# Performance work log

Hardware: AMD Instinct MI355X
Metric: run time of the kernel (lower is better)

## Reference

```python
import jax, jax.numpy as jnp
import numpy as np

GRID_H = 128
GRID_W = 128
D = 64
K = 16
HID = 4 * D
EPS = 1e-5


def _hankel_filters(L, k):
    # Hankel matrix Z[i,j] = 2 / ((i+j)^3 - (i+j)), 1-indexed; top-k eigvecs scaled by eigval^0.25
    idx = np.arange(1, L + 1)
    s = (idx[:, None] + idx[None, :]).astype(np.float64)
    Z = 2.0 / (s ** 3 - s)
    vals, vecs = np.linalg.eigh(Z)
    phi = vecs[:, -k:] * (vals[-k:] ** 0.25)
    return jnp.asarray(phi, dtype=jnp.float32)  # (L, k)


def setup_inputs() -> dict:
    key = jax.random.key(0)
    ks = jax.random.split(key, 9)
    def n(k, shape, scale=0.02):
        return jax.random.normal(k, shape, dtype=jnp.float32) * scale
    return {
        'v': jax.random.normal(ks[0], (4, GRID_H * GRID_W, D), dtype=jnp.float32),
        'gamma_row': jnp.ones((D,), jnp.float32), 'beta_row': jnp.zeros((D,), jnp.float32),
        'gamma_col': jnp.ones((D,), jnp.float32), 'beta_col': jnp.zeros((D,), jnp.float32),
        'm_plus_row': n(ks[1], (K, D, D)), 'm_minus_row': n(ks[2], (K, D, D)),
        'm_plus_col': n(ks[3], (K, D, D)), 'm_minus_col': n(ks[4], (K, D, D)),
        'w1_row': n(ks[5], (D, HID)), 'b1_row': jnp.zeros((HID,), jnp.float32),
        'w2_row': n(ks[6], (HID, D)), 'b2_row': jnp.zeros((D,), jnp.float32),
        'w1_col': n(ks[7], (D, HID)), 'b1_col': jnp.zeros((HID,), jnp.float32),
        'w2_col': n(ks[8], (HID, D)), 'b2_col': jnp.zeros((D,), jnp.float32),
        'phi_row': _hankel_filters(GRID_W, K),
        'phi_col': _hankel_filters(GRID_H, K),
    }


def _layernorm(x, g, b):
    mu = jnp.mean(x, -1, keepdims=True)
    var = jnp.mean((x - mu) ** 2, -1, keepdims=True)
    return (x - mu) * jax.lax.rsqrt(var + EPS) * g + b


def _ministu(x, phi, mp, mm, w1, b1, w2, b2):
    # x: (B, L, d); phi: (L, K). Causal FFT conv with pos/neg featurization, then per-filter projection + MLP.
    B, L, d = x.shape
    nfft = 2 * L
    sgn = jnp.where(jnp.arange(L) % 2 == 0, 1.0, -1.0).astype(x.dtype)  # (-1)^t
    pf = jnp.fft.rfft(phi, n=nfft, axis=0)                         # (F, K)
    xf = jnp.fft.rfft(x, n=nfft, axis=1)                           # (B, F, d)
    xmf = jnp.fft.rfft(x * sgn[None, :, None], n=nfft, axis=1)     # (B, F, d)
    up = jnp.fft.irfft(pf[None, :, :, None] * xf[:, :, None, :], n=nfft, axis=1)[:, :L]   # (B, L, K, d)
    um = jnp.fft.irfft(pf[None, :, :, None] * xmf[:, :, None, :], n=nfft, axis=1)[:, :L]
    um = um * sgn[None, :, None, None]
    spec = jnp.einsum('blkd,kde->ble', up, mp) + jnp.einsum('blkd,kde->ble', um, mm)
    h = jax.nn.gelu(spec @ w1 + b1)
    return h @ w2 + b2


def reference(v, gamma_row, beta_row, gamma_col, beta_col,
              m_plus_row, m_minus_row, m_plus_col, m_minus_col,
              w1_row, b1_row, w2_row, b2_row,
              w1_col, b1_col, w2_col, b2_col,
              phi_row, phi_col):
    B, N, d = v.shape
    x = v.reshape(B, GRID_H, GRID_W, d)
    # row pass: (B*H, W, d)
    xr = x.reshape(B * GRID_H, GRID_W, d)
    xr = xr + _ministu(_layernorm(xr, gamma_row, beta_row), phi_row,
                       m_plus_row, m_minus_row, w1_row, b1_row, w2_row, b2_row)
    x = xr.reshape(B, GRID_H, GRID_W, d).transpose(0, 2, 1, 3)
    # col pass: (B*W, H, d)
    xc = x.reshape(B * GRID_W, GRID_H, d)
    xc = xc + _ministu(_layernorm(xc, gamma_col, beta_col), phi_col,
                       m_plus_col, m_minus_col, w1_col, b1_col, w2_col, b2_col)
    x = xc.reshape(B, GRID_W, GRID_H, d).transpose(0, 2, 1, 3)
    return x.reshape(B, N, d)
```

## Files before the change

kernel.cpp:

```cpp
#include <hip/hip_runtime.h>
#include <hip/hip_fp8.h>

typedef __attribute__((ext_vector_type(8))) short bf16x8;
typedef __attribute__((ext_vector_type(4))) float f32x4;
typedef __attribute__((ext_vector_type(8))) int i32x8;
typedef __attribute__((ext_vector_type(4))) unsigned int u32x4;

__device__ __forceinline__ float gelu_fast(float x) {
    const float u = 0.7978845608028654f * x * (1.0f + 0.044715f * x * x);
    return x * __builtin_amdgcn_rcpf(1.0f + __expf(-2.0f * u));
}

__device__ __forceinline__ unsigned short f2bf(float x) {
    union { float f; unsigned int u; } v; v.f = x;
    unsigned int r = v.u + 0x7FFF + ((v.u >> 16) & 1);
    return (unsigned short)(r >> 16);
}

__device__ __forceinline__ unsigned char f2fp8(float x) {
    __hip_fp8_e4m3 h(x);
    return *(unsigned char*)&h;
}

__global__ __launch_bounds__(256) void init_kernel(const float* __restrict__ phi_r, const float* __restrict__ mp_r,
                                                   const float* __restrict__ mm_r, unsigned char* __restrict__ GfR,
                                                   const float* __restrict__ phi_c, const float* __restrict__ mp_c,
                                                   const float* __restrict__ mm_c, unsigned char* __restrict__ GfC,
                                                   const float* __restrict__ w1r, const float* __restrict__ w1c,
                                                   const float* __restrict__ w2r, const float* __restrict__ w2c,
                                                   unsigned short* __restrict__ w1tr, unsigned short* __restrict__ w1tc,
                                                   unsigned short* __restrict__ w2tr, unsigned short* __restrict__ w2tc) {
    const int bid = blockIdx.x, tid = threadIdx.x;
    __shared__ float phis[256];
    __shared__ unsigned char tile8[4096];
    if (bid < 256) {
        const int side = bid >> 7, rem = bid & 127;
        const int chunk = rem >> 3, s0 = (rem & 7) * 16;
        const float* phi = side ? phi_c : phi_r;
        const float* mp  = side ? mp_c  : mp_r;
        const float* mm  = side ? mm_c  : mm_r;
        unsigned char* Gf8 = side ? GfC : GfR;
        const int i = chunk * 256 + tid;
        float pe[16], po[16];
#pragma unroll
        for (int k = 0; k < 16; ++k) {
            const float a = mp[k * 4096 + i];
            const float b = mm[k * 4096 + i];
            pe[k] = a + b; po[k] = a - b;
        }
        phis[tid] = phi[s0 * 16 + tid];
        __syncthreads();
        const int e = tid & 63, dl = tid >> 6;
        const int d0 = chunk * 4;
#pragma unroll
        for (int sb = 0; sb < 16; ++sb) {
            const int s = s0 + sb;
            const float* pk = &phis[sb * 16];
            float acc = 0.0f;
            if (s & 1) {
#pragma unroll
                for (int k = 0; k < 16; ++k) acc += pk[k] * po[k];
            } else {
#pragma unroll
                for (int k = 0; k < 16; ++k) acc += pk[k] * pe[k];
            }
            tile8[sb * 256 + e * 4 + dl] = f2fp8(acc * 32.0f);
        }
        __syncthreads();
#pragma unroll
        for (int it = 0; it < 4; ++it) {
            const int p = it * 256 + tid;
            const int sb = p >> 6, ee = p & 63;
            unsigned int v = *(const unsigned int*)&tile8[sb * 256 + ee * 4];
            const int s = s0 + sb;
            const int sp = s >> 1, hi = s & 1;
            const int k0 = 64 * hi + d0;
            const int gg = k0 >> 5, kk0 = k0 & 31;
            *(unsigned int*)&Gf8[(size_t)sp * 8192 + (ee >> 4) * 2048 +
                                 ((ee & 15) + 16 * gg) * 32 + kk0] = v;
        }
    } else {
        const int b = bid - 256;
        if (b < 2) {
            const float* w1 = b ? w1c : w1r;
            unsigned short* dst = b ? w1tc : w1tr;
            const int n = tid;
            for (int k = 0; k < 64; ++k) dst[n * 64 + k] = f2bf(w1[k * 256 + n]);
        } else {
            const float* w2 = (b == 3) ? w2c : w2r;
            unsigned short* dst = (b == 3) ? w2tc : w2tr;
            const int n = tid & 63, kq = tid >> 6;
            for (int kk2 = 0; kk2 < 64; ++kk2) {
                const int k = kq * 64 + kk2;
                dst[n * 256 + k] = f2bf(w2[k * 64 + n]);
            }
        }
    }
}

#define SPEC_BODY(RR, BC, BN)                                                        \
    {                                                                                \
        const int sp_ = 4 * (RR) + w;                                                \
        if ((RR) < 15) {                                                             \
            const unsigned char* gq = Gf8 + (size_t)(sp_ + 4) * 8192 + lane * 32;    \
            _Pragma("unroll")                                                        \
            for (int f = 0; f < 4; ++f) BN[f] = *(const i32x8*)(gq + f * 2048);      \
        }                                                                            \
        const int jmin_ = __builtin_amdgcn_readfirstlane((2 * sp_ + 1) >> 4);        \
        __builtin_amdgcn_s_setprio(1);                                               \
        _Pragma("unroll")                                                            \
        for (int j = 0; j < 8; ++j) {                                                \
            if (j >= jmin_) {                                                        \
                const int srow = 16 + 16 * j - 2 * sp_ - (g >> 1) + m;               \
                const int cb_ = 2 * (g & 1);                                         \
                u32x4 lo_ = *(const u32x4*)&lds8[srow * 64 + ((cb_ ^ (srow & 3)) << 4)];       \
                u32x4 hi_ = *(const u32x4*)&lds8[srow * 64 + (((cb_ + 1) ^ (srow & 3)) << 4)]; \
                i32x8 av;                                                            \
                av[0] = lo_[0]; av[1] = lo_[1]; av[2] = lo_[2]; av[3] = lo_[3];      \
                av[4] = hi_[0]; av[5] = hi_[1]; av[6] = hi_[2]; av[7] = hi_[3];      \
                _Pragma("unroll")                                                    \
                for (int nt = 0; nt < 4; ++nt)                                       \
                    acc[j][nt] = __builtin_amdgcn_mfma_scale_f32_16x16x128_f8f6f4(   \
                        av, BC[nt], acc[j][nt], 0, 0, 0, 0x7F7F7F7F, 0, 0x7F7F7F7F); \
            }                                                                        \
        }                                                                            \
        __builtin_amdgcn_s_setprio(0);                                               \
    }

__global__ __launch_bounds__(256, 2) void fused_kernel(const float* __restrict__ xin,
                                                       float* __restrict__ xout,
                                                       const unsigned char* __restrict__ Gf8,
                                                       const unsigned short* __restrict__ w1t,
                                                       const unsigned short* __restrict__ w2t,
                                                       const float* __restrict__ b1,
                                                       const float* __restrict__ b2,
                                                       const float* __restrict__ gamma,
                                                       const float* __restrict__ beta,
                                                       int rmul, int tmul) {
    __shared__ unsigned char lds8[51200];
    unsigned short* const ldsu = (unsigned short*)lds8;
    const int tid = threadIdx.x;
    const int w = tid >> 6, lane = tid & 63;
    const int seq = blockIdx.x;
    const int m = lane & 15, g = lane >> 4;
    const int bb = seq >> 7, rr = seq & 127;
    const size_t base = (size_t)bb * 1048576 + (size_t)rr * (size_t)rmul;

    *(unsigned int*)&lds8[tid * 4] = 0u;

    i32x8 Ba[4], Bb[4];
    {
        const unsigned char* gq = Gf8 + (size_t)w * 8192 + lane * 32;
#pragma unroll
        for (int f = 0; f < 4; ++f) Ba[f] = *(const i32x8*)(gq + f * 2048);
    }

    {
        const float gl = gamma[lane], bl = beta[lane];
        float xv[32];
#pragma unroll
        for (int ti = 0; ti < 32; ++ti)
            xv[ti] = xin[base + (size_t)(w * 32 + ti) * tmul + lane];
#pragma unroll
        for (int ti = 0; ti < 32; ++ti) {
            const int t = w * 32 + ti;
            float s1 = xv[ti];
#pragma unroll
            for (int mm2 = 32; mm2 >= 1; mm2 >>= 1) s1 += __shfl_xor(s1, mm2);
            const float mu = s1 * (1.0f / 64.0f);
            const float dv = xv[ti] - mu;
            float s2 = dv * dv;
#pragma unroll
            for (int mm2 = 32; mm2 >= 1; mm2 >>= 1) s2 += __shfl_xor(s2, mm2);
            const float rstd = rsqrtf(s2 * (1.0f / 64.0f) + 1e-5f);
            const float nv = dv * rstd * gl + bl;
            lds8[(t + 16) * 64 + (((lane >> 4) ^ (t & 3)) << 4) + (lane & 15)] = f2fp8(nv);
        }
    }
    __syncthreads();

    f32x4 acc[8][4];
#pragma unroll
    for (int j = 0; j < 8; ++j)
#pragma unroll
        for (int nt = 0; nt < 4; ++nt) {
            f32x4 z = {0.0f, 0.0f, 0.0f, 0.0f};
            acc[j][nt] = z;
        }
    for (int rp = 0; rp < 8; ++rp) {
        SPEC_BODY(2 * rp,     Ba, Bb);
        SPEC_BODY(2 * rp + 1, Bb, Ba);
    }

    char* const scrA = (char*)lds8 + 18432;
    char* const scrB = (char*)lds8 + 34816;
    if (w == 1 || w == 3) {
        char* pb = (w == 1 ? scrA : scrB) + lane * 16;
#pragma unroll
        for (int j = 0; j < 4; ++j)
#pragma unroll
            for (int nt = 0; nt < 4; ++nt)
                *(f32x4*)(pb + (j * 4 + nt) * 1024) = acc[j][nt];
    }
    bf16x8 bw1a[2][2], bw1b[2][2];
    float b1va[2], b1vb[2];
#pragma unroll
    for (int nt = 0; nt < 2; ++nt) {
        const int col0 = w * 32 + nt * 16 + m;
#pragma unroll
        for (int j = 0; j < 2; ++j) {
            bw1a[nt][j] = *(const bf16x8*)&w1t[col0 * 64 + (4 * j + g) * 8];
            bw1b[nt][j] = *(const bf16x8*)&w1t[(128 + col0) * 64 + (4 * j + g) * 8];
        }
        b1va[nt] = b1[col0];
        b1vb[nt] = b1[128 + col0];
    }
    __syncthreads();
    if (w == 0 || w == 2) {
        const char* pb = (w == 0 ? scrA : scrB) + lane * 16;
#pragma unroll
        for (int j = 0; j < 4; ++j)
#pragma unroll
            for (int nt = 0; nt < 4; ++nt)
                acc[j][nt] += *(const f32x4*)(pb + (j * 4 + nt) * 1024);
    }
    __syncthreads();
    if (w == 1 || w == 3) {
        char* pb = (w == 1 ? scrA : scrB) + lane * 16;
#pragma unroll
        for (int j = 4; j < 8; ++j)
#pragma unroll
            for (int nt = 0; nt < 4; ++nt)
                *(f32x4*)(pb + ((j - 4) * 4 + nt) * 1024) = acc[j][nt];
    }
    __syncthreads();
    if (w == 0 || w == 2) {
        const char* pb = (w == 0 ? scrA : scrB) + lane * 16;
#pragma unroll
        for (int j = 4; j < 8; ++j)
#pragma unroll
            for (int nt = 0; nt < 4; ++nt)
                acc[j][nt] += *(const f32x4*)(pb + ((j - 4) * 4 + nt) * 1024);
        if (w == 0) {
#pragma unroll
            for (int j = 4; j < 8; ++j)
#pragma unroll
                for (int nt = 0; nt < 4; ++nt)
                    *(f32x4*)(scrA + ((j - 4) * 4 + nt) * 1024 + lane * 16) = acc[j][nt];
        } else {
#pragma unroll
            for (int j = 0; j < 4; ++j)
#pragma unroll
                for (int nt = 0; nt < 4; ++nt)
                    *(f32x4*)(scrB + (j * 4 + nt) * 1024 + lane * 16) = acc[j][nt];
        }
    }
    __syncthreads();
    if (w == 0) {
#pragma unroll
        for (int j = 0; j < 4; ++j)
#pragma unroll
            for (int nt = 0; nt < 4; ++nt) {
                acc[j][nt] += *(const f32x4*)(scrB + (j * 4 + nt) * 1024 + lane * 16);
#pragma unroll
                for (int rv = 0; rv < 4; ++rv) {
                    const int row = j * 16 + 4 * g + rv;
                    const int col = nt * 16 + m;
                    ldsu[row * 64 + (((col >> 3) ^ (row & 7)) << 3) + (col & 7)] = f2bf(acc[j][nt][rv] * 0.03125f);
                }
            }
    } else if (w == 2) {
#pragma unroll
        for (int j = 4; j < 8; ++j)
#pragma unroll
            for (int nt = 0; nt < 4; ++nt) {
                acc[j][nt] += *(const f32x4*)(scrA + ((j - 4) * 4 + nt) * 1024 + lane * 16);
#pragma unroll
                for (int rv = 0; rv < 4; ++rv) {
                    const int row = j * 16 + 4 * g + rv;
                    const int col = nt * 16 + m;
                    ldsu[row * 64 + (((col >> 3) ^ (row & 7)) << 3) + (col & 7)] = f2bf(acc[j][nt][rv] * 0.03125f);
                }
            }
    }
    __syncthreads();

    float xr[2][4][4];
#pragma unroll
    for (int mt = 0; mt < 2; ++mt)
#pragma unroll
        for (int nt = 0; nt < 4; ++nt)
#pragma unroll
            for (int rv = 0; rv < 4; ++rv)
                xr[mt][nt][rv] = xin[base + (size_t)((w + 4 * mt) * 16 + 4 * g + rv) * tmul + nt * 16 + m];

    float b2v[4];
#pragma unroll
    for (int nt = 0; nt < 4; ++nt) b2v[nt] = b2[nt * 16 + m];
    f32x4 acc2[2][4];
#pragma unroll
    for (int mt = 0; mt < 2; ++mt)
#pragma unroll
        for (int nt = 0; nt < 4; ++nt) {
            f32x4 z = {b2v[nt], b2v[nt], b2v[nt], b2v[nt]};
            acc2[mt][nt] = z;
        }

#pragma unroll
    for (int half = 0; half < 2; ++half) {
        f32x4 acc1[8][2];
#pragma unroll
        for (int mt = 0; mt < 8; ++mt)
#pragma unroll
            for (int nt = 0; nt < 2; ++nt) {
                const float bv = half ? b1vb[nt] : b1va[nt];
                f32x4 z = {bv, bv, bv, bv};
                acc1[mt][nt] = z;
            }
        __builtin_amdgcn_s_setprio(1);
#pragma unroll
        for (int mt = 0; mt < 8; ++mt) {
            const int row = mt * 16 + m;
            const int c0 = (g ^ (row & 7)) << 3;
            bf16x8 a0 = *(const bf16x8*)&ldsu[row * 64 + c0];
            bf16x8 a1 = *(const bf16x8*)&ldsu[row * 64 + (c0 ^ 32)];
#pragma unroll
            for (int nt = 0; nt < 2; ++nt) {
                const bf16x8 w0f = half ? bw1b[nt][0] : bw1a[nt][0];
                const bf16x8 w1f = half ? bw1b[nt][1] : bw1a[nt][1];
                acc1[mt][nt] = __builtin_amdgcn_mfma_f32_16x16x32_bf16(a0, w0f, acc1[mt][nt], 0, 0, 0);
                acc1[mt][nt] = __builtin_amdgcn_mfma_f32_16x16x32_bf16(a1, w1f, acc1[mt][nt], 0, 0, 0);
            }
        }
        __builtin_amdgcn_s_setprio(0);
#pragma unroll
        for (int mt = 0; mt < 8; ++mt)
#pragma unroll
            for (int nt = 0; nt < 2; ++nt) {
                const int col = w * 32 + nt * 16 + m;
                const int c = col >> 3, jj = col & 7;
#pragma unroll
                for (int rv = 0; rv < 4; ++rv) {
                    const int row = mt * 16 + 4 * g + rv;
                    ldsu[8192 + row * 128 + ((c ^ (row & 7)) << 3) + jj] = f2bf(gelu_fast(acc1[mt][nt][rv]));
                }
            }
        __syncthreads();

        __builtin_amdgcn_s_setprio(1);
#pragma unroll
        for (int j = 0; j < 4; ++j) {
            bf16x8 aa[2];
#pragma unroll
            for (int mt = 0; mt < 2; ++mt) {
                const int row = (w + 4 * mt) * 16 + m;
                aa[mt] = *(const bf16x8*)&ldsu[8192 + row * 128 + (((4 * j + g) ^ (row & 7)) << 3)];
            }
#pragma unroll
            for (int nt = 0; nt < 4; ++nt) {
                const int row = nt * 16 + m;
                bf16x8 bfr = *(const bf16x8*)&w2t[row * 256 + half * 128 + (4 * j + g) * 8];
                acc2[0][nt] = __builtin_amdgcn_mfma_f32_16x16x32_bf16(aa[0], bfr, acc2[0][nt], 0, 0, 0);
                acc2[1][nt] = __builtin_amdgcn_mfma_f32_16x16x32_bf16(aa[1], bfr, acc2[1][nt], 0, 0, 0);
            }
        }
        __builtin_amdgcn_s_setprio(0);
        if (half == 0) __syncthreads();
    }

#pragma unroll
    for (int mt = 0; mt < 2; ++mt)
#pragma unroll
        for (int nt = 0; nt < 4; ++nt)
#pragma unroll
            for (int rv = 0; rv < 4; ++rv) {
                const int row = (w + 4 * mt) * 16 + 4 * g + rv;
                const int col = nt * 16 + m;
                const size_t xi = base + (size_t)row * tmul + col;
                xout[xi] = xr[mt][nt][rv] + acc2[mt][nt][rv];
            }
}

extern "C" void kernel_launch(void* const* d_in, const int* in_sizes, int n_in,
                              void* d_out, int out_size, void* d_ws, size_t ws_size,
                              hipStream_t stream) {
    const float* v         = (const float*)d_in[0];
    const float* gamma_row = (const float*)d_in[1];
    const float* beta_row  = (const float*)d_in[2];
    const float* gamma_col = (const float*)d_in[3];
    const float* beta_col  = (const float*)d_in[4];
    const float* mp_row    = (const float*)d_in[5];
    const float* mm_row    = (const float*)d_in[6];
    const float* mp_col    = (const float*)d_in[7];
    const float* mm_col    = (const float*)d_in[8];
    const float* w1_row    = (const float*)d_in[9];
    const float* b1_row    = (const float*)d_in[10];
    const float* w2_row    = (const float*)d_in[11];
    const float* b2_row    = (const float*)d_in[12];
    const float* w1_col    = (const float*)d_in[13];
    const float* b1_col    = (const float*)d_in[14];
    const float* w2_col    = (const float*)d_in[15];
    const float* b2_col    = (const float*)d_in[16];
    const float* phi_row   = (const float*)d_in[17];
    const float* phi_col   = (const float*)d_in[18];
    float* out = (float*)d_out;
    char* ws   = (char*)d_ws;

    unsigned char* GfR   = (unsigned char*)ws;
    unsigned char* GfC   = (unsigned char*)(ws + (1u << 20));
    unsigned short* w1tR = (unsigned short*)(ws + (2u << 20));
    unsigned short* w2tR = (unsigned short*)(ws + (2u << 20) + 32768);
    unsigned short* w1tC = (unsigned short*)(ws + (2u << 20) + 65536);
    unsigned short* w2tC = (unsigned short*)(ws + (2u << 20) + 98304);

    init_kernel<<<260, 256, 0, stream>>>(phi_row, mp_row, mm_row, GfR,
                                         phi_col, mp_col, mm_col, GfC,
                                         w1_row, w1_col, w2_row, w2_col,
                                         w1tR, w1tC, w2tR, w2tC);

    fused_kernel<<<512, 256, 0, stream>>>(v, out, GfR, w1tR, w2tR, b1_row, b2_row,
                                          gamma_row, beta_row, 8192, 64);
    fused_kernel<<<512, 256, 0, stream>>>(out, out, GfC, w1tC, w2tC, b1_col, b2_col,
                                          gamma_col, beta_col, 64, 8192);
}
```

Before: 100.1 us.

## Partition spectral MFMA work by output row tiles instead of filter slices

Each wave now owns two output row tiles (w and 7-w) and loops over all filter positions sp needed for those rows, rather than splitting the sp range across waves and accumulating all eight tiles. This removes the multi-stage cross-wave LDS reduction, several barriers and the 8x4 accumulator array, which cuts register pressure. The pairing of a short and a long tile is meant to balance the triangular causal work across waves. Each wave now loads all G slices itself, so global/L2 traffic for the fp8 filter operands goes up.

```diff
diff --git a/kernel.cpp b/kernel.cpp
--- a/kernel.cpp
+++ b/kernel.cpp
@@ -98,31 +98,40 @@
     }
 }
 
-#define SPEC_BODY(RR, BC, BN)                                                        \
+#define SPEC_BODY(SP, BC, BN)                                                        \
     {                                                                                \
-        const int sp_ = 4 * (RR) + w;                                                \
-        if ((RR) < 15) {                                                             \
-            const unsigned char* gq = Gf8 + (size_t)(sp_ + 4) * 8192 + lane * 32;    \
+        const int sp_ = (SP);                                                        \
+        if (sp_ + 2 <= spmax) {                                                      \
+            const unsigned char* gq = Gf8 + (size_t)(sp_ + 2) * 8192 + lane * 32;    \
             _Pragma("unroll")                                                        \
             for (int f = 0; f < 4; ++f) BN[f] = *(const i32x8*)(gq + f * 2048);      \
         }                                                                            \
-        const int jmin_ = __builtin_amdgcn_readfirstlane((2 * sp_ + 1) >> 4);        \
         __builtin_amdgcn_s_setprio(1);                                               \
-        _Pragma("unroll")                                                            \
-        for (int j = 0; j < 8; ++j) {                                                \
-            if (j >= jmin_) {                                                        \
-                const int srow = 16 + 16 * j - 2 * sp_ - (g >> 1) + m;               \
-                const int cb_ = 2 * (g & 1);                                         \
-                u32x4 lo_ = *(const u32x4*)&lds8[srow * 64 + ((cb_ ^ (srow & 3)) << 4)];       \
-                u32x4 hi_ = *(const u32x4*)&lds8[srow * 64 + (((cb_ + 1) ^ (srow & 3)) << 4)]; \
-                i32x8 av;                                                            \
-                av[0] = lo_[0]; av[1] = lo_[1]; av[2] = lo_[2]; av[3] = lo_[3];      \
-                av[4] = hi_[0]; av[5] = hi_[1]; av[6] = hi_[2]; av[7] = hi_[3];      \
-                _Pragma("unroll")                                                    \
-                for (int nt = 0; nt < 4; ++nt)                                       \
-                    acc[j][nt] = __builtin_amdgcn_mfma_scale_f32_16x16x128_f8f6f4(   \
-                        av, BC[nt], acc[j][nt], 0, 0, 0, 0x7F7F7F7F, 0, 0x7F7F7F7F); \
-            }                                                                        \
+        {                                                                            \
+            const int srow = 16 + 16 * j2 - 2 * sp_ - (g >> 1) + m;                  \
+            const int cb_ = 2 * (g & 1);                                             \
+            u32x4 lo_ = *(const u32x4*)&lds8[srow * 64 + ((cb_ ^ (srow & 3)) << 4)];       \
+            u32x4 hi_ = *(const u32x4*)&lds8[srow * 64 + (((cb_ + 1) ^ (srow & 3)) << 4)]; \
+            i32x8 av;                                                                \
+            av[0] = lo_[0]; av[1] = lo_[1]; av[2] = lo_[2]; av[3] = lo_[3];          \
+            av[4] = hi_[0]; av[5] = hi_[1]; av[6] = hi_[2]; av[7] = hi_[3];          \
+            _Pragma("unroll")                                                        \
+            for (int nt = 0; nt < 4; ++nt)                                           \
+                acc[1][nt] = __builtin_amdgcn_mfma_scale_f32_16x16x128_f8f6f4(       \
+                    av, BC[nt], acc[1][nt], 0, 0, 0, 0x7F7F7F7F, 0, 0x7F7F7F7F);     \
+        }                                                                            \
+        if (sp_ <= 8 * w + 7) {                                                      \
+            const int srow = 16 + 16 * w - 2 * sp_ - (g >> 1) + m;                   \
+            const int cb_ = 2 * (g & 1);                                             \
+            u32x4 lo_ = *(const u32x4*)&lds8[srow * 64 + ((cb_ ^ (srow & 3)) << 4)];       \
+            u32x4 hi_ = *(const u32x4*)&lds8[srow * 64 + (((cb_ + 1) ^ (srow & 3)) << 4)]; \
+            i32x8 av;                                                                \
+            av[0] = lo_[0]; av[1] = lo_[1]; av[2] = lo_[2]; av[3] = lo_[3];          \
+            av[4] = hi_[0]; av[5] = hi_[1]; av[6] = hi_[2]; av[7] = hi_[3];          \
+            _Pragma("unroll")                                                        \
+            for (int nt = 0; nt < 4; ++nt)                                           \
+                acc[0][nt] = __builtin_amdgcn_mfma_scale_f32_16x16x128_f8f6f4(       \
+                    av, BC[nt], acc[0][nt], 0, 0, 0, 0x7F7F7F7F, 0, 0x7F7F7F7F);     \
         }                                                                            \
         __builtin_amdgcn_s_setprio(0);                                               \
     }
@@ -137,7 +146,7 @@
                                                        const float* __restrict__ gamma,
                                                        const float* __restrict__ beta,
                                                        int rmul, int tmul) {
-    __shared__ unsigned char lds8[51200];
+    __shared__ unsigned char lds8[49152];
     unsigned short* const ldsu = (unsigned short*)lds8;
     const int tid = threadIdx.x;
     const int w = tid >> 6, lane = tid & 63;
@@ -145,14 +154,18 @@
     const int m = lane & 15, g = lane >> 4;
     const int bb = seq >> 7, rr = seq & 127;
     const size_t base = (size_t)bb * 1048576 + (size_t)rr * (size_t)rmul;
+    const int j2 = 7 - w;
+    const int spmax = 8 * j2 + 7;
 
     *(unsigned int*)&lds8[tid * 4] = 0u;
 
     i32x8 Ba[4], Bb[4];
     {
-        const unsigned char* gq = Gf8 + (size_t)w * 8192 + lane * 32;
+        const unsigned char* gq = Gf8 + lane * 32;
 #pragma unroll
         for (int f = 0; f < 4; ++f) Ba[f] = *(const i32x8*)(gq + f * 2048);
+#pragma unroll
+        for (int f = 0; f < 4; ++f) Bb[f] = *(const i32x8*)(gq + 8192 + f * 2048);
     }
 
     {
@@ -179,29 +192,20 @@
     }
     __syncthreads();
 
-    f32x4 acc[8][4];
-#pragma unroll
-    for (int j = 0; j < 8; ++j)
+    f32x4 acc[2][4];
+#pragma unroll
+    for (int jt = 0; jt < 2; ++jt)
 #pragma unroll
         for (int nt = 0; nt < 4; ++nt) {
             f32x4 z = {0.0f, 0.0f, 0.0f, 0.0f};
-            acc[j][nt] = z;
-        }
-    for (int rp = 0; rp < 8; ++rp) {
+            acc[jt][nt] = z;
+        }
+    const int nrp = (spmax + 1) >> 1;
+    for (int rp = 0; rp < nrp; ++rp) {
         SPEC_BODY(2 * rp,     Ba, Bb);
         SPEC_BODY(2 * rp + 1, Bb, Ba);
     }
 
-    char* const scrA = (char*)lds8 + 18432;
-    char* const scrB = (char*)lds8 + 34816;
-    if (w == 1 || w == 3) {
-        char* pb = (w == 1 ? scrA : scrB) + lane * 16;
-#pragma unroll
-        for (int j = 0; j < 4; ++j)
-#pragma unroll
-            for (int nt = 0; nt < 4; ++nt)
-                *(f32x4*)(pb + (j * 4 + nt) * 1024) = acc[j][nt];
-    }
     bf16x8 bw1a[2][2], bw1b[2][2];
     float b1va[2], b1vb[2];
 #pragma unroll
@@ -216,71 +220,17 @@
         b1vb[nt] = b1[128 + col0];
     }
     __syncthreads();
-    if (w == 0 || w == 2) {
-        const char* pb = (w == 0 ? scrA : scrB) + lane * 16;
-#pragma unroll
-        for (int j = 0; j < 4; ++j)
-#pragma unroll
-            for (int nt = 0; nt < 4; ++nt)
-                acc[j][nt] += *(const f32x4*)(pb + (j * 4 + nt) * 1024);
-    }
-    __syncthreads();
-    if (w == 1 || w == 3) {
-        char* pb = (w == 1 ? scrA : scrB) + lane * 16;
-#pragma unroll
-        for (int j = 4; j < 8; ++j)
-#pragma unroll
-            for (int nt = 0; nt < 4; ++nt)
-                *(f32x4*)(pb + ((j - 4) * 4 + nt) * 1024) = acc[j][nt];
-    }
-    __syncthreads();
-    if (w == 0 || w == 2) {
-        const char* pb = (w == 0 ? scrA : scrB) + lane * 16;
-#pragma unroll
-        for (int j = 4; j < 8; ++j)
-#pragma unroll
-            for (int nt = 0; nt < 4; ++nt)
-                acc[j][nt] += *(const f32x4*)(pb + ((j - 4) * 4 + nt) * 1024);
-        if (w == 0) {
-#pragma unroll
-            for (int j = 4; j < 8; ++j)
-#pragma unroll
-                for (int nt = 0; nt < 4; ++nt)
-                    *(f32x4*)(scrA + ((j - 4) * 4 + nt) * 1024 + lane * 16) = acc[j][nt];
-        } else {
-#pragma unroll
-            for (int j = 0; j < 4; ++j)
-#pragma unroll
-                for (int nt = 0; nt < 4; ++nt)
-                    *(f32x4*)(scrB + (j * 4 + nt) * 1024 + lane * 16) = acc[j][nt];
-        }
-    }
-    __syncthreads();
-    if (w == 0) {
-#pragma unroll
-        for (int j = 0; j < 4; ++j)
-#pragma unroll
-            for (int nt = 0; nt < 4; ++nt) {
-                acc[j][nt] += *(const f32x4*)(scrB + (j * 4 + nt) * 1024 + lane * 16);
-#pragma unroll
-                for (int rv = 0; rv < 4; ++rv) {
-                    const int row = j * 16 + 4 * g + rv;
-                    const int col = nt * 16 + m;
-                    ldsu[row * 64 + (((col >> 3) ^ (row & 7)) << 3) + (col & 7)] = f2bf(acc[j][nt][rv] * 0.03125f);
-                }
-            }
-    } else if (w == 2) {
-#pragma unroll
-        for (int j = 4; j < 8; ++j)
-#pragma unroll
-            for (int nt = 0; nt < 4; ++nt) {
-                acc[j][nt] += *(const f32x4*)(scrA + ((j - 4) * 4 + nt) * 1024 + lane * 16);
-#pragma unroll
-                for (int rv = 0; rv < 4; ++rv) {
-                    const int row = j * 16 + 4 * g + rv;
-                    const int col = nt * 16 + m;
-                    ldsu[row * 64 + (((col >> 3) ^ (row & 7)) << 3) + (col & 7)] = f2bf(acc[j][nt][rv] * 0.03125f);
-                }
+
+#pragma unroll
+    for (int jt = 0; jt < 2; ++jt) {
+        const int j = jt ? j2 : w;
+#pragma unroll
+        for (int nt = 0; nt < 4; ++nt)
+#pragma unroll
+            for (int rv = 0; rv < 4; ++rv) {
+                const int row = j * 16 + 4 * g + rv;
+                const int col = nt * 16 + m;
+                ldsu[row * 64 + (((col >> 3) ^ (row & 7)) << 3) + (col & 7)] = f2bf(acc[jt][nt][rv] * 0.03125f);
             }
     }
     __syncthreads();
```

Result: slower. 124.0 us (+23.9%).
